# Optimization experiments

Hardware: AMD Instinct MI355X
Metric: run time of the kernel (lower is better)

## Reference

```python
import jax, jax.numpy as jnp
import numpy as np

N_NODES = 100000
N_EDGES = 3200000
IN_DIM = 512
HID_DIM = 16


def spmm(edge_src, edge_dst, edge_weight, feats):
    # out[i] = sum_{(j->i) in E} w_e * feats[j]  (sparse adj @ feats)
    gathered = feats[edge_src] * edge_weight[:, None]  # [E, D]
    return jax.ops.segment_sum(gathered, edge_dst, num_segments=N_NODES)


def setup_inputs() -> dict:
    key = jax.random.key(0)
    ks = jax.random.split(key, 8)
    x = jax.random.normal(ks[0], (N_NODES, IN_DIM), dtype=jnp.float32)
    edge_src = jax.random.randint(ks[1], (N_EDGES,), 0, N_NODES, dtype=jnp.int32)
    edge_dst = jax.random.randint(ks[2], (N_EDGES,), 0, N_NODES, dtype=jnp.int32)
    # normalized adjacency weights (positive, small, like D^-1/2 A D^-1/2 entries)
    edge_weight = jax.random.uniform(ks[3], (N_EDGES,), dtype=jnp.float32) * 0.1
    # Glorot-style init for GraphConvolution weights
    W1 = jax.random.normal(ks[4], (IN_DIM, HID_DIM), dtype=jnp.float32) * (1.0 / np.sqrt(IN_DIM))
    b1 = jnp.zeros((HID_DIM,), dtype=jnp.float32)
    W2 = jax.random.normal(ks[5], (HID_DIM, 1), dtype=jnp.float32) * (1.0 / np.sqrt(HID_DIM))
    b2 = jnp.zeros((1,), dtype=jnp.float32)
    return {"x": x, "edge_src": edge_src, "edge_dst": edge_dst,
            "edge_weight": edge_weight, "W1": W1, "b1": b1, "W2": W2, "b2": b2}


def reference(x, edge_src, edge_dst, edge_weight, W1, b1, W2, b2):
    # Layer 1: GraphConvolution(input_dim -> hidden_dim) + ReLU
    h = spmm(edge_src, edge_dst, edge_weight, x @ W1) + b1  # [N, 16]
    h = jax.nn.relu(h)
    # dropout is identity in eval mode (training=False)
    # Layer 2: GraphConvolution(hidden_dim -> 1)
    out = spmm(edge_src, edge_dst, edge_weight, h @ W2) + b2  # [N, 1]
    return out
```

## Files before the change

kernel.cpp:

```cpp
#include <hip/hip_runtime.h>
#include <hip/hip_fp16.h>

#define N_NODES 100000
#define N_EDGES 3200000
#define IN_DIM  512
#define HID_DIM 16

#define B_BKT   782
#define BKT_SH  7
#define EPB     12500
#define CAP_MAX 4608

__device__ __forceinline__ void atomic_add_f32(float* p, float v) {
    __hip_atomic_fetch_add(p, v, __ATOMIC_RELAXED, __HIP_MEMORY_SCOPE_AGENT);
}
__device__ __forceinline__ int atomic_add_i32(int* p, int v) {
    return __hip_atomic_fetch_add(p, v, __ATOMIC_RELAXED, __HIP_MEMORY_SCOPE_AGENT);
}

__global__ void z0_init(int* __restrict__ cursor, int cap) {
    int b = blockIdx.x * blockDim.x + threadIdx.x;
    if (b < B_BKT) cursor[b] = b * cap;
}

__global__ __launch_bounds__(256) void g1_xw(const float* __restrict__ x,
                                             const float* __restrict__ W1,
                                             __half* __restrict__ xwh) {
    const int lane  = threadIdx.x & 63;
    const int wave  = (blockIdx.x * blockDim.x + threadIdx.x) >> 6;
    const int nwave = (gridDim.x * blockDim.x) >> 6;

    float w[8][16];
#pragma unroll
    for (int q = 0; q < 8; ++q) {
        int k = (q < 4) ? (lane * 4 + q) : (256 + lane * 4 + (q - 4));
        const float4* wr = (const float4*)(W1 + (size_t)k * HID_DIM);
        float4 a = wr[0], b = wr[1], c = wr[2], d = wr[3];
        w[q][0]=a.x; w[q][1]=a.y; w[q][2]=a.z; w[q][3]=a.w;
        w[q][4]=b.x; w[q][5]=b.y; w[q][6]=b.z; w[q][7]=b.w;
        w[q][8]=c.x; w[q][9]=c.y; w[q][10]=c.z; w[q][11]=c.w;
        w[q][12]=d.x; w[q][13]=d.y; w[q][14]=d.z; w[q][15]=d.w;
    }

    const float4* x4 = (const float4*)x;
    int row = wave;
    float4 xa, xb;
    if (row < N_NODES) {
        xa = x4[(size_t)row * 128 + lane];
        xb = x4[(size_t)row * 128 + 64 + lane];
    }
    while (row < N_NODES) {
        int nrow = row + nwave;
        float4 na, nb;
        if (nrow < N_NODES) {
            na = x4[(size_t)nrow * 128 + lane];
            nb = x4[(size_t)nrow * 128 + 64 + lane];
        }
        float acc[16];
#pragma unroll
        for (int j = 0; j < 16; ++j) {
            acc[j] = xa.x * w[0][j] + xa.y * w[1][j] + xa.z * w[2][j] + xa.w * w[3][j]
                   + xb.x * w[4][j] + xb.y * w[5][j] + xb.z * w[6][j] + xb.w * w[7][j];
        }
#pragma unroll
        for (int j = 0; j < 16; ++j) {
            acc[j] += __shfl_xor(acc[j], 32);
            acc[j] += __shfl_xor(acc[j], 16);
        }
        float c8[8];
#pragma unroll
        for (int i = 0; i < 8; ++i) {
            bool hi = (lane & 8) != 0;
            float keep = hi ? acc[i + 8] : acc[i];
            float send = hi ? acc[i] : acc[i + 8];
            c8[i] = keep + __shfl_xor(send, 8);
        }
        float c4[4];
#pragma unroll
        for (int i = 0; i < 4; ++i) {
            bool hi = (lane & 4) != 0;
            float keep = hi ? c8[i + 4] : c8[i];
            float send = hi ? c8[i] : c8[i + 4];
            c4[i] = keep + __shfl_xor(send, 4);
        }
        float c2[2];
#pragma unroll
        for (int i = 0; i < 2; ++i) {
            bool hi = (lane & 2) != 0;
            float keep = hi ? c4[i + 2] : c4[i];
            float send = hi ? c4[i] : c4[i + 2];
            c2[i] = keep + __shfl_xor(send, 2);
        }
        {
            bool hi = (lane & 1) != 0;
            float keep = hi ? c2[1] : c2[0];
            float send = hi ? c2[0] : c2[1];
            float c1 = keep + __shfl_xor(send, 1);
            if (lane < 16) xwh[(size_t)row * HID_DIM + lane] = __float2half_rn(c1);
        }
        row = nrow; xa = na; xb = nb;
    }
}

__global__ __launch_bounds__(1024) void s1_bin(const int* __restrict__ src,
                                               const int* __restrict__ dst,
                                               const float* __restrict__ wgt,
                                               int* __restrict__ cursor,
                                               uint2* __restrict__ rec, int cap) {
    __shared__ int hist[B_BKT];
    __shared__ int base[B_BKT];
    const int t = threadIdx.x;
    for (int b = t; b < B_BKT; b += 1024) hist[b] = 0;
    __syncthreads();
    const int e0 = blockIdx.x * EPB;
    const int4*   d4 = (const int4*)(dst + e0);
    const int4*   s4 = (const int4*)(src + e0);
    const float4* w4 = (const float4*)(wgt + e0);
    const int NG = EPB / 4;
    for (int g = t; g < NG; g += 1024) {
        int4 d = d4[g];
        atomicAdd(&hist[d.x >> BKT_SH], 1);
        atomicAdd(&hist[d.y >> BKT_SH], 1);
        atomicAdd(&hist[d.z >> BKT_SH], 1);
        atomicAdd(&hist[d.w >> BKT_SH], 1);
    }
    __syncthreads();
    for (int b = t; b < B_BKT; b += 1024) {
        int c = hist[b];
        base[b] = c > 0 ? atomic_add_i32(&cursor[b], c) : 0;
    }
    __syncthreads();
    for (int b = t; b < B_BKT; b += 1024) hist[b] = 0;
    __syncthreads();
    for (int g = t; g < NG; g += 1024) {
        int4 d = d4[g];
        int4 s = s4[g];
        float4 w = w4[g];
        {
            int b = d.x >> BKT_SH;
            int pos = base[b] + atomicAdd(&hist[b], 1);
            rec[pos] = make_uint2(((unsigned)s.x << BKT_SH) | (unsigned)(d.x & 127),
                                  __float_as_uint(w.x));
        }
        {
            int b = d.y >> BKT_SH;
            int pos = base[b] + atomicAdd(&hist[b], 1);
            rec[pos] = make_uint2(((unsigned)s.y << BKT_SH) | (unsigned)(d.y & 127),
                                  __float_as_uint(w.y));
        }
        {
            int b = d.z >> BKT_SH;
            int pos = base[b] + atomicAdd(&hist[b], 1);
            rec[pos] = make_uint2(((unsigned)s.z << BKT_SH) | (unsigned)(d.z & 127),
                                  __float_as_uint(w.z));
        }
        {
            int b = d.w >> BKT_SH;
            int pos = base[b] + atomicAdd(&hist[b], 1);
            rec[pos] = make_uint2(((unsigned)s.w << BKT_SH) | (unsigned)(d.w & 127),
                                  __float_as_uint(w.w));
        }
    }
}

__global__ __launch_bounds__(512) void s2_sort(const int* __restrict__ cursor,
                                               uint2* __restrict__ rec,
                                               int2* __restrict__ row, int cap) {
    __shared__ uint2 srec[CAP_MAX];
    __shared__ int ocnt[128], scn[128], cur[128];
    const int t = threadIdx.x;
    const int bkt = blockIdx.x;
    const int e0 = bkt * cap;
    int n = cursor[bkt] - e0;
    n = max(0, min(n, cap));
    if (t < 128) ocnt[t] = 0;
    __syncthreads();
    for (int i = t; i < n; i += 512) {
        uint2 r = rec[e0 + i];
        srec[i] = r;
        atomicAdd(&ocnt[r.x & 127u], 1);
    }
    __syncthreads();
    if (t < 128) scn[t] = ocnt[t];
    __syncthreads();
    for (int off = 1; off < 128; off <<= 1) {
        int v = 0;
        if (t < 128 && t >= off) v = scn[t - off];
        __syncthreads();
        if (t < 128 && t >= off) scn[t] += v;
        __syncthreads();
    }
    if (t < 128) {
        int b = scn[t] - ocnt[t];
        cur[t] = b;
        int node = (bkt << BKT_SH) + t;
        if (node < N_NODES) row[node] = make_int2(e0 + b, ocnt[t]);
    }
    __syncthreads();
    for (int i = t; i < n; i += 512) {
        uint2 r = srec[i];
        int d = (int)(r.x & 127u);
        int pos = atomicAdd(&cur[d], 1);
        rec[e0 + pos] = make_uint2(r.x >> BKT_SH, r.y);
    }
}

__global__ __launch_bounds__(256) void p4_layer1(const int2* __restrict__ row,
                                                 const uint2* __restrict__ rec,
                                                 const __half* __restrict__ xwh,
                                                 const float* __restrict__ b1,
                                                 const float* __restrict__ W2,
                                                 float* __restrict__ hw) {
    const int t = threadIdx.x;
    const int node = blockIdx.x * 16 + (t >> 4);
    const int j = t & 15;
    int2 r = row[node];
    int e = r.x;
    const int end = r.x + r.y;
    float acc = 0.0f;
    for (; e + 4 <= end; e += 4) {
        uint2 q0 = rec[e], q1 = rec[e + 1], q2 = rec[e + 2], q3 = rec[e + 3];
        float f0 = __half2float(xwh[(size_t)q0.x * HID_DIM + j]);
        float f1 = __half2float(xwh[(size_t)q1.x * HID_DIM + j]);
        float f2 = __half2float(xwh[(size_t)q2.x * HID_DIM + j]);
        float f3 = __half2float(xwh[(size_t)q3.x * HID_DIM + j]);
        acc += __uint_as_float(q0.y) * f0;
        acc += __uint_as_float(q1.y) * f1;
        acc += __uint_as_float(q2.y) * f2;
        acc += __uint_as_float(q3.y) * f3;
    }
    for (; e < end; ++e) {
        uint2 q = rec[e];
        acc += __uint_as_float(q.y) * __half2float(xwh[(size_t)q.x * HID_DIM + j]);
    }
    float v = fmaxf(acc + b1[j], 0.0f) * W2[j];
    v += __shfl_xor(v, 1);
    v += __shfl_xor(v, 2);
    v += __shfl_xor(v, 4);
    v += __shfl_xor(v, 8);
    if (j == 0) hw[node] = v;
}

__global__ __launch_bounds__(256) void p5_layer2(const int2* __restrict__ row,
                                                 const uint2* __restrict__ rec,
                                                 const float* __restrict__ hwv,
                                                 const float* __restrict__ b2,
                                                 float* __restrict__ out) {
    const int t = threadIdx.x;
    const int node = blockIdx.x * 32 + (t >> 3);
    const int i = t & 7;
    int2 r = row[node];
    const int end = r.x + r.y;
    int k = r.x + i;
    float s = 0.0f;
    for (; k + 24 < end; k += 32) {
        uint2 a = rec[k], b = rec[k + 8], c = rec[k + 16], d = rec[k + 24];
        float ha = hwv[a.x], hb = hwv[b.x], hc = hwv[c.x], hd = hwv[d.x];
        s += __uint_as_float(a.y) * ha + __uint_as_float(b.y) * hb
           + __uint_as_float(c.y) * hc + __uint_as_float(d.y) * hd;
    }
    for (; k < end; k += 8) {
        uint2 a = rec[k];
        s += __uint_as_float(a.y) * hwv[a.x];
    }
    s += __shfl_xor(s, 1);
    s += __shfl_xor(s, 2);
    s += __shfl_xor(s, 4);
    if (i == 0) out[node] = b2[0] + s;
}

__global__ void f0_zero(float* __restrict__ h, const float* __restrict__ b2,
                        float* __restrict__ out) {
    int i = blockIdx.x * blockDim.x + threadIdx.x;
    if (i < N_NODES * HID_DIM) h[i] = 0.0f;
    if (i < N_NODES) out[i] = b2[0];
}
__global__ void k2_spmm1(const int* __restrict__ src, const int* __restrict__ dst,
                         const float* __restrict__ wgt, const __half* __restrict__ xwh,
                         float* __restrict__ h) {
    int t = blockIdx.x * blockDim.x + threadIdx.x;
    int e = t >> 4;
    int j = t & (HID_DIM - 1);
    if (e < N_EDGES) {
        float v = wgt[e] * __half2float(xwh[(size_t)src[e] * HID_DIM + j]);
        atomic_add_f32(&h[(size_t)dst[e] * HID_DIM + j], v);
    }
}
__global__ void k3_act(const float* __restrict__ h, const float* __restrict__ b1,
                       const float* __restrict__ W2, float* __restrict__ hw) {
    int i = blockIdx.x * blockDim.x + threadIdx.x;
    if (i >= N_NODES) return;
    const float4* h4 = (const float4*)(h + (size_t)i * HID_DIM);
    const float4* b4 = (const float4*)b1;
    const float4* w4 = (const float4*)W2;
    float acc = 0.0f;
#pragma unroll
    for (int q = 0; q < HID_DIM / 4; ++q) {
        float4 hv = h4[q]; float4 bv = b4[q]; float4 wv = w4[q];
        acc += fmaxf(hv.x + bv.x, 0.0f) * wv.x;
        acc += fmaxf(hv.y + bv.y, 0.0f) * wv.y;
        acc += fmaxf(hv.z + bv.z, 0.0f) * wv.z;
        acc += fmaxf(hv.w + bv.w, 0.0f) * wv.w;
    }
    hw[i] = acc;
}
__global__ void k4_spmm2(const int* __restrict__ src, const int* __restrict__ dst,
                         const float* __restrict__ wgt, const float* __restrict__ hw,
                         float* __restrict__ out) {
    int e = blockIdx.x * blockDim.x + threadIdx.x;
    if (e < N_EDGES) atomic_add_f32(&out[dst[e]], wgt[e] * hw[src[e]]);
}


extern "C" void kernel_launch(void* const* d_in, const int* in_sizes, int n_in,
                              void* d_out, int out_size, void* d_ws, size_t ws_size,
                              hipStream_t stream) {
    const float* x    = (const float*)d_in[0];
    const int*   esrc = (const int*)  d_in[1];
    const int*   edst = (const int*)  d_in[2];
    const float* ew   = (const float*)d_in[3];
    const float* W1   = (const float*)d_in[4];
    const float* b1   = (const float*)d_in[5];
    const float* W2   = (const float*)d_in[6];
    const float* b2   = (const float*)d_in[7];
    float* out = (float*)d_out;
    char* ws = (char*)d_ws;

    __half* xwh    = (__half*)ws;
    float*  hw     = (float*)(ws + (size_t)N_NODES * HID_DIM * 2);
    int*    cursor = (int*)(hw + N_NODES);
    int2*   row    = (int2*)(((size_t)(cursor + B_BKT) + 7) & ~(size_t)7);
    size_t rec_off = ((size_t)((char*)(row + N_NODES) - ws) + 15) & ~(size_t)15;
    uint2* rec = (uint2*)(ws + rec_off);

    int cap = 0;
    if (ws_size > rec_off) {
        size_t cap_fit = (ws_size - rec_off) / ((size_t)B_BKT * sizeof(uint2));
        cap = (int)(cap_fit < CAP_MAX ? cap_fit : CAP_MAX);
    }

    if (cap >= 4480) {
        z0_init<<<(B_BKT + 255) / 256, 256, 0, stream>>>(cursor, cap);
        g1_xw<<<3125, 256, 0, stream>>>(x, W1, xwh);
        s1_bin<<<N_EDGES / EPB, 1024, 0, stream>>>(esrc, edst, ew, cursor, rec, cap);
        s2_sort<<<B_BKT, 512, 0, stream>>>(cursor, rec, row, cap);
        p4_layer1<<<N_NODES / 16, 256, 0, stream>>>(row, rec, xwh, b1, W2, hw);
        p5_layer2<<<N_NODES / 32, 256, 0, stream>>>(row, rec, hw, b2, out);
    } else {
        __half* f_xwh = (__half*)ws;
        float*  f_h   = (float*)(ws + (size_t)N_NODES * HID_DIM * 2);
        float*  f_hw  = f_h + (size_t)N_NODES * HID_DIM;
        int n = N_NODES * HID_DIM;
        f0_zero<<<(n + 255) / 256, 256, 0, stream>>>(f_h, b2, out);
        g1_xw<<<3125, 256, 0, stream>>>(x, W1, f_xwh);
        k2_spmm1<<<(N_EDGES * 16) / 256, 256, 0, stream>>>(esrc, edst, ew, f_xwh, f_h);
        k3_act<<<(N_NODES + 255) / 256, 256, 0, stream>>>(f_h, b1, W2, f_hw);
        k4_spmm2<<<(N_EDGES + 255) / 256, 256, 0, stream>>>(esrc, edst, ew, f_hw, out);
    }
}
```

Measured before the change: 479.8 us.

## Compute X@W1 with split-bf16 MFMA instead of FP32 FMA with shuffle reductions

Replaces the persistent-wave FP32 dense projection, which ended in a long shuffle reduction, with an MFMA 16x16x32 bf16 kernel. Each wave computes one 16-row tile. W1 is split into hi/lo bf16 parts held in shared memory, and x is split per element on the fly. Three MFMAs per k-chunk (hi*hi, lo*hi, hi*lo) approximate FP32 accuracy. The kernel reads 200MB of x and is likely memory-bound, so the gain depends on whether the old ALU and shuffle work was limiting. The new access pattern also reads 32B segments per row across lanes, which may coalesce less well.

Result: faster. 444.9 us (-7.3%).

```diff
diff --git a/kernel.cpp b/kernel.cpp
--- a/kernel.cpp
+++ b/kernel.cpp
@@ -11,11 +11,21 @@
 #define EPB     12500
 #define CAP_MAX 4608
 
+#define G1_TILES 6250
+
+typedef __attribute__((ext_vector_type(8))) short bf16x8;
+typedef __attribute__((ext_vector_type(4))) float f32x4;
+
 __device__ __forceinline__ void atomic_add_f32(float* p, float v) {
     __hip_atomic_fetch_add(p, v, __ATOMIC_RELAXED, __HIP_MEMORY_SCOPE_AGENT);
 }
 __device__ __forceinline__ int atomic_add_i32(int* p, int v) {
     return __hip_atomic_fetch_add(p, v, __ATOMIC_RELAXED, __HIP_MEMORY_SCOPE_AGENT);
+}
+
+__device__ __forceinline__ unsigned short bf16_rne(float f) {
+    unsigned u = __float_as_uint(f);
+    return (unsigned short)((u + 0x7fffu + ((u >> 16) & 1u)) >> 16);
 }
 
 __global__ void z0_init(int* __restrict__ cursor, int cap) {
@@ -23,83 +33,68 @@
     if (b < B_BKT) cursor[b] = b * cap;
 }
 
-__global__ __launch_bounds__(256) void g1_xw(const float* __restrict__ x,
-                                             const float* __restrict__ W1,
-                                             __half* __restrict__ xwh) {
-    const int lane  = threadIdx.x & 63;
-    const int wave  = (blockIdx.x * blockDim.x + threadIdx.x) >> 6;
-    const int nwave = (gridDim.x * blockDim.x) >> 6;
-
-    float w[8][16];
+__global__ __launch_bounds__(256) void g1_xw_mfma(const float* __restrict__ x,
+                                                  const float* __restrict__ W1,
+                                                  __half* __restrict__ xwh) {
+    __shared__ alignas(16) unsigned short whi[16 * 64 * 8];
+    __shared__ alignas(16) unsigned short wlo[16 * 64 * 8];
+    const int t = threadIdx.x;
+
+    for (int idx = t; idx < 16 * 64 * 8; idx += 256) {
+        int c  = idx >> 9;
+        int l  = (idx >> 3) & 63;
+        int tt = idx & 7;
+        int k  = c * 32 + ((l >> 4) << 3) + tt;
+        int j  = l & 15;
+        float w = W1[k * HID_DIM + j];
+        unsigned u = __float_as_uint(w);
+        float hif = __uint_as_float(u & 0xffff0000u);
+        whi[idx] = (unsigned short)(u >> 16);
+        wlo[idx] = bf16_rne(w - hif);
+    }
+    __syncthreads();
+
+    const int lane = t & 63;
+    const int wid  = blockIdx.x * 4 + (t >> 6);
+    if (wid >= G1_TILES) return;
+    const int row0 = wid * 16;
+
+    const float* xrow = x + (size_t)(row0 + (lane & 15)) * IN_DIM + ((lane >> 4) << 3);
+    const unsigned short* whp = &whi[lane * 8];
+    const unsigned short* wlp = &wlo[lane * 8];
+
+    f32x4 acc = {0.f, 0.f, 0.f, 0.f};
+    float4 a0 = *(const float4*)(xrow);
+    float4 a1 = *(const float4*)(xrow + 4);
 #pragma unroll
-    for (int q = 0; q < 8; ++q) {
-        int k = (q < 4) ? (lane * 4 + q) : (256 + lane * 4 + (q - 4));
-        const float4* wr = (const float4*)(W1 + (size_t)k * HID_DIM);
-        float4 a = wr[0], b = wr[1], c = wr[2], d = wr[3];
-        w[q][0]=a.x; w[q][1]=a.y; w[q][2]=a.z; w[q][3]=a.w;
-        w[q][4]=b.x; w[q][5]=b.y; w[q][6]=b.z; w[q][7]=b.w;
-        w[q][8]=c.x; w[q][9]=c.y; w[q][10]=c.z; w[q][11]=c.w;
-        w[q][12]=d.x; w[q][13]=d.y; w[q][14]=d.z; w[q][15]=d.w;
-    }
-
-    const float4* x4 = (const float4*)x;
-    int row = wave;
-    float4 xa, xb;
-    if (row < N_NODES) {
-        xa = x4[(size_t)row * 128 + lane];
-        xb = x4[(size_t)row * 128 + 64 + lane];
-    }
-    while (row < N_NODES) {
-        int nrow = row + nwave;
-        float4 na, nb;
-        if (nrow < N_NODES) {
-            na = x4[(size_t)nrow * 128 + lane];
-            nb = x4[(size_t)nrow * 128 + 64 + lane];
-        }
-        float acc[16];
+    for (int c = 0; c < 16; ++c) {
+        float4 n0, n1;
+        if (c < 15) {
+            n0 = *(const float4*)(xrow + (c + 1) * 32);
+            n1 = *(const float4*)(xrow + (c + 1) * 32 + 4);
+        }
+        float av[8] = {a0.x, a0.y, a0.z, a0.w, a1.x, a1.y, a1.z, a1.w};
+        bf16x8 ah, al;
 #pragma unroll
-        for (int j = 0; j < 16; ++j) {
-            acc[j] = xa.x * w[0][j] + xa.y * w[1][j] + xa.z * w[2][j] + xa.w * w[3][j]
-                   + xb.x * w[4][j] + xb.y * w[5][j] + xb.z * w[6][j] + xb.w * w[7][j];
-        }
+        for (int e = 0; e < 8; ++e) {
+            unsigned u = __float_as_uint(av[e]);
+            ah[e] = (short)(u >> 16);
+            float lof = av[e] - __uint_as_float(u & 0xffff0000u);
+            al[e] = (short)bf16_rne(lof);
+        }
+        bf16x8 bh = *(const bf16x8*)(whp + (size_t)c * 512);
+        bf16x8 bl = *(const bf16x8*)(wlp + (size_t)c * 512);
+        acc = __builtin_amdgcn_mfma_f32_16x16x32_bf16(ah, bh, acc, 0, 0, 0);
+        acc = __builtin_amdgcn_mfma_f32_16x16x32_bf16(al, bh, acc, 0, 0, 0);
+        acc = __builtin_amdgcn_mfma_f32_16x16x32_bf16(ah, bl, acc, 0, 0, 0);
+        a0 = n0; a1 = n1;
+    }
+
+    const int n     = lane & 15;
+    const int rbase = row0 + ((lane >> 4) << 2);
 #pragma unroll
-        for (int j = 0; j < 16; ++j) {
-            acc[j] += __shfl_xor(acc[j], 32);
-            acc[j] += __shfl_xor(acc[j], 16);
-        }
-        float c8[8];
-#pragma unroll
-        for (int i = 0; i < 8; ++i) {
-            bool hi = (lane & 8) != 0;
-            float keep = hi ? acc[i + 8] : acc[i];
-            float send = hi ? acc[i] : acc[i + 8];
-            c8[i] = keep + __shfl_xor(send, 8);
-        }
-        float c4[4];
-#pragma unroll
-        for (int i = 0; i < 4; ++i) {
-            bool hi = (lane & 4) != 0;
-            float keep = hi ? c8[i + 4] : c8[i];
-            float send = hi ? c8[i] : c8[i + 4];
-            c4[i] = keep + __shfl_xor(send, 4);
-        }
-        float c2[2];
-#pragma unroll
-        for (int i = 0; i < 2; ++i) {
-            bool hi = (lane & 2) != 0;
-            float keep = hi ? c4[i + 2] : c4[i];
-            float send = hi ? c4[i] : c4[i + 2];
-            c2[i] = keep + __shfl_xor(send, 2);
-        }
-        {
-            bool hi = (lane & 1) != 0;
-            float keep = hi ? c2[1] : c2[0];
-            float send = hi ? c2[0] : c2[1];
-            float c1 = keep + __shfl_xor(send, 1);
-            if (lane < 16) xwh[(size_t)row * HID_DIM + lane] = __float2half_rn(c1);
-        }
-        row = nrow; xa = na; xb = nb;
-    }
+    for (int i = 0; i < 4; ++i)
+        xwh[(size_t)(rbase + i) * HID_DIM + n] = __float2half_rn(acc[i]);
 }
 
 __global__ __launch_bounds__(1024) void s1_bin(const int* __restrict__ src,
@@ -341,7 +336,7 @@
 
     if (cap >= 4480) {
         z0_init<<<(B_BKT + 255) / 256, 256, 0, stream>>>(cursor, cap);
-        g1_xw<<<3125, 256, 0, stream>>>(x, W1, xwh);
+        g1_xw_mfma<<<(G1_TILES + 3) / 4, 256, 0, stream>>>(x, W1, xwh);
         s1_bin<<<N_EDGES / EPB, 1024, 0, stream>>>(esrc, edst, ew, cursor, rec, cap);
         s2_sort<<<B_BKT, 512, 0, stream>>>(cursor, rec, row, cap);
         p4_layer1<<<N_NODES / 16, 256, 0, stream>>>(row, rec, xwh, b1, W2, hw);
@@ -352,7 +347,7 @@
         float*  f_hw  = f_h + (size_t)N_NODES * HID_DIM;
         int n = N_NODES * HID_DIM;
         f0_zero<<<(n + 255) / 256, 256, 0, stream>>>(f_h, b2, out);
-        g1_xw<<<3125, 256, 0, stream>>>(x, W1, f_xwh);
+        g1_xw_mfma<<<(G1_TILES + 3) / 4, 256, 0, stream>>>(x, W1, f_xwh);
         k2_spmm1<<<(N_EDGES * 16) / 256, 256, 0, stream>>>(esrc, edst, ew, f_xwh, f_h);
         k3_act<<<(N_NODES + 255) / 256, 256, 0, stream>>>(f_h, b1, W2, f_hw);
         k4_spmm2<<<(N_EDGES + 255) / 256, 256, 0, stream>>>(esrc, edst, ew, f_hw, out);
```
